# Performance work log

Measured on AMD Instinct MI355X. Metric: run time of the kernel, lower is better.

## Reference

```python
import jax, jax.numpy as jnp
import numpy as np

N_PER_G = 18
GRAPHS = 4096
N = GRAPHS * N_PER_G            # 73728 nodes
E = GRAPHS * N_PER_G * (N_PER_G - 1)  # 1253376 edges (fully connected per graph)
F_IN = 1536                     # sfreq * timestep
EPS = 1e-5
SLOPE = 0.01


def _lrelu(v):
    return jnp.where(v >= 0, v, SLOPE * v)


def setup_inputs() -> dict:
    key = jax.random.key(0)
    ks = jax.random.split(key, 32)
    # node features
    x = jax.random.normal(ks[0], (N, F_IN), dtype=jnp.float32)
    # fully-connected edges within each 18-node graph
    src, dst = np.meshgrid(np.arange(N_PER_G), np.arange(N_PER_G), indexing='ij')
    m = src != dst
    src, dst = src[m], dst[m]                      # [306]
    offs = (np.arange(GRAPHS) * N_PER_G)[:, None]
    row = (offs + src[None, :]).reshape(-1)
    col = (offs + dst[None, :]).reshape(-1)
    edge_index = jnp.asarray(np.stack([row, col]), dtype=jnp.int32)  # [2,E]
    edge_weight = jax.random.uniform(ks[1], (E,), dtype=jnp.float32)
    batch = jnp.asarray(np.arange(N) // N_PER_G, dtype=jnp.int32)

    def lin(k, fi, fo):
        kw, kb = jax.random.split(k)
        s = 1.0 / np.sqrt(fi)
        W = jax.random.uniform(kw, (fi, fo), jnp.float32, -s, s)
        b = jax.random.uniform(kb, (fo,), jnp.float32, -s, s)
        return W, b

    def bn(k, f):
        k1, k2 = jax.random.split(k)
        g = jnp.ones((f,), jnp.float32)
        be = jnp.zeros((f,), jnp.float32)
        rm = jax.random.normal(k1, (f,), jnp.float32) * 0.1
        rv = jax.random.uniform(k2, (f,), jnp.float32) + 0.5
        return g, be, rm, rv

    W1, b1 = lin(ks[2], F_IN, 32)
    W2, b2 = lin(ks[3], 32, 64)
    W3, b3 = lin(ks[4], 64, 128)
    g1, be1, rm1, rv1 = bn(ks[5], 32)
    g2, be2, rm2, rv2 = bn(ks[6], 64)
    g3, be3, rm3, rv3 = bn(ks[7], 128)
    fW1, fb1 = lin(ks[8], 128, 64)
    fW2, fb2 = lin(ks[9], 64, 32)
    fW3, fb3 = lin(ks[10], 32, 16)
    fW4, fb4 = lin(ks[11], 16, 1)

    return dict(x=x, edge_index=edge_index, edge_weight=edge_weight, batch=batch,
                W1=W1, b1=b1, g1=g1, be1=be1, rm1=rm1, rv1=rv1,
                W2=W2, b2=b2, g2=g2, be2=be2, rm2=rm2, rv2=rv2,
                W3=W3, b3=b3, g3=g3, be3=be3, rm3=rm3, rv3=rv3,
                fW1=fW1, fb1=fb1, fW2=fW2, fb2=fb2,
                fW3=fW3, fb3=fb3, fW4=fW4, fb4=fb4)


def _gcn_norm(edge_index, edge_weight):
    # add self loops (weight 1), symmetric normalization (PyG GCNConv, improved=False)
    row = jnp.concatenate([edge_index[0], jnp.arange(N, dtype=edge_index.dtype)])
    col = jnp.concatenate([edge_index[1], jnp.arange(N, dtype=edge_index.dtype)])
    w = jnp.concatenate([edge_weight, jnp.ones((N,), edge_weight.dtype)])
    deg = jax.ops.segment_sum(w, col, num_segments=N)
    dinv = jnp.where(deg > 0, jax.lax.rsqrt(jnp.maximum(deg, 1e-30)), 0.0)
    norm = dinv[row] * w * dinv[col]
    return row, col, norm


def _gcn(x, W, b, row, col, norm):
    h = x @ W                                       # [N, Fout]
    out = jax.ops.segment_sum(norm[:, None] * h[row], col, num_segments=N)
    return out + b


def _bn(h, g, be, rm, rv):
    return (h - rm) * jax.lax.rsqrt(rv + EPS) * g + be


def reference(x, edge_index, edge_weight, batch,
              W1, b1, g1, be1, rm1, rv1,
              W2, b2, g2, be2, rm2, rv2,
              W3, b3, g3, be3, rm3, rv3,
              fW1, fb1, fW2, fb2, fW3, fb3, fW4, fb4):
    row, col, norm = _gcn_norm(edge_index, edge_weight)
    h = _lrelu(_bn(_gcn(x, W1, b1, row, col, norm), g1, be1, rm1, rv1))
    h = _lrelu(_bn(_gcn(h, W2, b2, row, col, norm), g2, be2, rm2, rv2))
    h = _lrelu(_bn(_gcn(h, W3, b3, row, col, norm), g3, be3, rm3, rv3))
    # global mean pool over graphs
    sums = jax.ops.segment_sum(h, batch, num_segments=GRAPHS)
    cnt = jax.ops.segment_sum(jnp.ones((N,), h.dtype), batch, num_segments=GRAPHS)
    h = sums / jnp.maximum(cnt, 1.0)[:, None]       # [G,128]
    # MLP head (dropout = identity in eval)
    h = _lrelu(h @ fW1 + fb1)
    h = _lrelu(h @ fW2 + fb2)
    h = _lrelu(h @ fW3 + fb3)
    h = h @ fW4 + fb4
    return h.squeeze(-1)                            # [G]
```

## Files before the change

kernel.cpp:

```cpp
#include <hip/hip_runtime.h>
#include <stdint.h>

#define GRAPHS 4096
#define NPG 18
#define EPERG 306
#define FIN 1536
#define BN_EPS 1e-5f
#define SLOPE 0.01f
#define GPB 8
#define RPB 144

using short8  = __attribute__((ext_vector_type(8))) short;
using ushort8 = __attribute__((ext_vector_type(8))) unsigned short;
using f32x4   = __attribute__((ext_vector_type(4))) float;

__device__ __forceinline__ unsigned short f2bf(float f) {
  unsigned u = __builtin_bit_cast(unsigned, f);
  u += 0x7fffu + ((u >> 16) & 1u);
  return (unsigned short)(u >> 16);
}

__device__ __forceinline__ short8 pack_bf16(const float4& a0, const float4& a1) {
  short8 af;
  af[0] = (short)f2bf(a0.x); af[1] = (short)f2bf(a0.y);
  af[2] = (short)f2bf(a0.z); af[3] = (short)f2bf(a0.w);
  af[4] = (short)f2bf(a1.x); af[5] = (short)f2bf(a1.y);
  af[6] = (short)f2bf(a1.z); af[7] = (short)f2bf(a1.w);
  return af;
}

__device__ __forceinline__ void wave_fence() {
  asm volatile("s_waitcnt lgkmcnt(0)" ::: "memory");
}

__global__ void prep_kernel(const float* __restrict__ W1,
    const float* __restrict__ b1, const float* __restrict__ g1,
    const float* __restrict__ be1, const float* __restrict__ rm1, const float* __restrict__ rv1,
    const float* __restrict__ b2, const float* __restrict__ g2,
    const float* __restrict__ be2, const float* __restrict__ rm2, const float* __restrict__ rv2,
    const float* __restrict__ b3, const float* __restrict__ g3,
    const float* __restrict__ be3, const float* __restrict__ rm3, const float* __restrict__ rv3,
    unsigned short* __restrict__ w1frag, float* __restrict__ ab) {
  const int tid = threadIdx.x;
  if (blockIdx.x < 24) {
    int slot = blockIdx.x * 256 + tid;
    int L  = slot & 63;
    int nt = (slot >> 6) & 1;
    int ks = slot >> 7;
    int n  = nt * 16 + (L & 15);
    int kb = ks * 32 + ((L >> 4) << 3);
    ushort8 v;
#pragma unroll
    for (int j = 0; j < 8; ++j) v[j] = f2bf(W1[(kb + j) * 32 + n]);
    *((ushort8*)w1frag + slot) = v;
  } else {
    if (tid < 32) {
      float a = g1[tid] * rsqrtf(rv1[tid] + BN_EPS);
      ab[tid] = a; ab[32 + tid] = (b1[tid] - rm1[tid]) * a + be1[tid];
    }
    if (tid < 64) {
      float a = g2[tid] * rsqrtf(rv2[tid] + BN_EPS);
      ab[64 + tid] = a; ab[128 + tid] = (b2[tid] - rm2[tid]) * a + be2[tid];
    }
    if (tid < 128) {
      float a = g3[tid] * rsqrtf(rv3[tid] + BN_EPS);
      ab[192 + tid] = a; ab[320 + tid] = (b3[tid] - rm3[tid]) * a + be3[tid];
    }
  }
}

__global__ __launch_bounds__(256, 2) void gcn_fused(
    const float* __restrict__ x, const float* __restrict__ ew,
    const unsigned short* __restrict__ w1frag, const float* __restrict__ ab,
    const float* __restrict__ W2, const float* __restrict__ W3,
    float* __restrict__ pooled) {
  const int bid  = blockIdx.x;
  const int tid  = threadIdx.x;
  const int lane = tid & 63;
  const int wv   = tid >> 6;

  __shared__ __align__(16) float P1[RPB][36];
  __shared__ float ew_s[GPB * EPERG];
  __shared__ float dinv_s[GPB][NPG];
  __shared__ float An_s[GPB][NPG][19];
  __shared__ __align__(16) float BufA[4][NPG][68];
  __shared__ __align__(16) float BufB[4][NPG][68];

  for (int i = tid; i < GPB * EPERG; i += 256)
    ew_s[i] = ew[(size_t)bid * (GPB * EPERG) + i];

  const int arow = lane & 15;
  const int akg  = lane >> 4;
  const short8* __restrict__ wf = (const short8*)w1frag + lane;
  const float* __restrict__ xg = x + (size_t)bid * RPB * FIN;
  float* __restrict__ PT = &BufA[0][0][0];

  for (int t = wv; t < 8; t += 4) {
    f32x4 acc0 = {0.f, 0.f, 0.f, 0.f};
    f32x4 acc1 = {0.f, 0.f, 0.f, 0.f};
    const float* __restrict__ xr = xg + (size_t)(t * 16 + arow) * FIN + (akg << 3);
#pragma unroll 4
    for (int ks = 0; ks < 48; ++ks) {
      float4 a0 = *(const float4*)(xr + ks * 32);
      float4 a1 = *(const float4*)(xr + ks * 32 + 4);
      short8 af = pack_bf16(a0, a1);
      acc0 = __builtin_amdgcn_mfma_f32_16x16x32_bf16(af, wf[(ks * 2 + 0) * 64], acc0, 0, 0, 0);
      acc1 = __builtin_amdgcn_mfma_f32_16x16x32_bf16(af, wf[(ks * 2 + 1) * 64], acc1, 0, 0, 0);
    }
    const int crow = t * 16 + (akg << 2);
#pragma unroll
    for (int q = 0; q < 4; ++q) {
      P1[crow + q][arow]      = acc0[q];
      P1[crow + q][arow + 16] = acc1[q];
    }
  }
  {
    f32x4 acc0 = {0.f, 0.f, 0.f, 0.f};
    f32x4 acc1 = {0.f, 0.f, 0.f, 0.f};
    const float* __restrict__ xr = xg + (size_t)(128 + arow) * FIN + (akg << 3);
    const int k0 = wv * 12;
#pragma unroll 4
    for (int ks = k0; ks < k0 + 12; ++ks) {
      float4 a0 = *(const float4*)(xr + ks * 32);
      float4 a1 = *(const float4*)(xr + ks * 32 + 4);
      short8 af = pack_bf16(a0, a1);
      acc0 = __builtin_amdgcn_mfma_f32_16x16x32_bf16(af, wf[(ks * 2 + 0) * 64], acc0, 0, 0, 0);
      acc1 = __builtin_amdgcn_mfma_f32_16x16x32_bf16(af, wf[(ks * 2 + 1) * 64], acc1, 0, 0, 0);
    }
#pragma unroll
    for (int q = 0; q < 4; ++q) {
      PT[wv * 1224 + ((akg << 2) + q) * 32 + arow]      = acc0[q];
      PT[wv * 1224 + ((akg << 2) + q) * 32 + arow + 16] = acc1[q];
    }
  }
  __syncthreads();

  if (tid < GPB * NPG) {
    int j = tid / NPG, d = tid - j * NPG;
    const float* e = ew_s + j * EPERG;
    float deg = 1.0f;
#pragma unroll
    for (int k = 0; k < 17; ++k) {
      int s = k + (k >= d);
      deg += e[s * 17 + (d - (d > s ? 1 : 0))];
    }
    dinv_s[j][d] = rsqrtf(deg);
  }
  for (int o = tid; o < 512; o += 256) {
    int r = o >> 5, c = o & 31;
    P1[128 + r][c] = PT[o] + PT[1224 + o] + PT[2448 + o] + PT[3672 + o];
  }
  __syncthreads();

  for (int o = tid; o < GPB * NPG * NPG; o += 256) {
    int j = o / (NPG * NPG), rm = o - j * (NPG * NPG);
    int d = rm / NPG, s = rm - d * NPG;
    float v;
    if (d == s) v = dinv_s[j][d] * dinv_s[j][d];
    else        v = dinv_s[j][s] * ew_s[j * EPERG + s * 17 + (d - (d > s ? 1 : 0))] * dinv_s[j][d];
    An_s[j][d][s] = v;
  }
  __syncthreads();

  float (*A_)[68] = BufA[wv];
  float (*B_)[68] = BufB[wv];

#pragma unroll 1
  for (int jj = 0; jj < 2; ++jj) {
    const int j = wv + (jj << 2);
    const float (*An)[19] = An_s[j];
    const float* P1g = &P1[j * NPG][0];

    for (int o4 = lane; o4 < 144; o4 += 64) {
      int d = o4 >> 3, cb = (o4 & 7) << 2;
      f32x4 s = {0.f, 0.f, 0.f, 0.f};
#pragma unroll
      for (int ss = 0; ss < NPG; ++ss) {
        float a = An[d][ss];
        f32x4 p = *(const f32x4*)(P1g + ss * 36 + cb);
        s[0] = fmaf(a, p[0], s[0]); s[1] = fmaf(a, p[1], s[1]);
        s[2] = fmaf(a, p[2], s[2]); s[3] = fmaf(a, p[3], s[3]);
      }
      f32x4 al = *(const f32x4*)(ab + cb), be = *(const f32x4*)(ab + 32 + cb);
#pragma unroll
      for (int q = 0; q < 4; ++q) {
        float v = fmaf(s[q], al[q], be[q]);
        s[q] = v >= 0.f ? v : SLOPE * v;
      }
      *(f32x4*)&A_[d][cb] = s;
    }
    wave_fence();

    for (int o4 = lane; o4 < 144; o4 += 64) {
      int d = o4 >> 3, cb = (o4 & 7) << 2;
      f32x4 s = {0.f, 0.f, 0.f, 0.f};
#pragma unroll
      for (int ss = 0; ss < NPG; ++ss) {
        float a = An[d][ss];
        f32x4 p = *(const f32x4*)&A_[ss][cb];
        s[0] = fmaf(a, p[0], s[0]); s[1] = fmaf(a, p[1], s[1]);
        s[2] = fmaf(a, p[2], s[2]); s[3] = fmaf(a, p[3], s[3]);
      }
      *(f32x4*)&B_[d][cb] = s;
    }
    wave_fence();

    {
      const float al = ab[64 + lane], be = ab[128 + lane];
      float w0 = W2[0 * 64 + lane], w1 = W2[1 * 64 + lane];
      float w2 = W2[2 * 64 + lane], w3 = W2[3 * 64 + lane];
      float s0=0.f,s1=0.f,s2=0.f,s3=0.f,s4=0.f,s5=0.f,s6=0.f,s7=0.f,s8=0.f;
      float s9=0.f,s10=0.f,s11=0.f,s12=0.f,s13=0.f,s14=0.f,s15=0.f,s16=0.f,s17=0.f;
#define L2_ROW(i) { f32x4 g = *(const f32x4*)&B_[i][k4 * 4]; \
        s##i = fmaf(g[0], w0, fmaf(g[1], w1, fmaf(g[2], w2, fmaf(g[3], w3, s##i)))); }
      for (int k4 = 0; k4 < 8; ++k4) {
        float n0 = 0.f, n1 = 0.f, n2 = 0.f, n3 = 0.f;
        if (k4 < 7) {
          n0 = W2[(k4 * 4 + 4) * 64 + lane]; n1 = W2[(k4 * 4 + 5) * 64 + lane];
          n2 = W2[(k4 * 4 + 6) * 64 + lane]; n3 = W2[(k4 * 4 + 7) * 64 + lane];
        }
        L2_ROW(0) L2_ROW(1) L2_ROW(2) L2_ROW(3) L2_ROW(4) L2_ROW(5)
        L2_ROW(6) L2_ROW(7) L2_ROW(8) L2_ROW(9) L2_ROW(10) L2_ROW(11)
        L2_ROW(12) L2_ROW(13) L2_ROW(14) L2_ROW(15) L2_ROW(16) L2_ROW(17)
        w0 = n0; w1 = n1; w2 = n2; w3 = n3;
      }
#undef L2_ROW
#define L2_OUT(i) { float v = fmaf(s##i, al, be); A_[i][lane] = v >= 0.f ? v : SLOPE * v; }
      L2_OUT(0) L2_OUT(1) L2_OUT(2) L2_OUT(3) L2_OUT(4) L2_OUT(5)
      L2_OUT(6) L2_OUT(7) L2_OUT(8) L2_OUT(9) L2_OUT(10) L2_OUT(11)
      L2_OUT(12) L2_OUT(13) L2_OUT(14) L2_OUT(15) L2_OUT(16) L2_OUT(17)
#undef L2_OUT
    }
    wave_fence();

    for (int o4 = lane; o4 < 288; o4 += 64) {
      int d = o4 >> 4, cb = (o4 & 15) << 2;
      f32x4 s = {0.f, 0.f, 0.f, 0.f};
#pragma unroll
      for (int ss = 0; ss < NPG; ++ss) {
        float a = An[d][ss];
        f32x4 p = *(const f32x4*)&A_[ss][cb];
        s[0] = fmaf(a, p[0], s[0]); s[1] = fmaf(a, p[1], s[1]);
        s[2] = fmaf(a, p[2], s[2]); s[3] = fmaf(a, p[3], s[3]);
      }
      *(f32x4*)&B_[d][cb] = s;
    }
    wave_fence();

    float pool0 = 0.f, pool1 = 0.f;
#pragma unroll 1
    for (int h = 0; h < 2; ++h) {
      const int cc = (h << 6) + lane;
      const float al = ab[192 + cc], be = ab[320 + cc];
      float w0 = W3[0 * 128 + cc], w1 = W3[1 * 128 + cc];
      float w2 = W3[2 * 128 + cc], w3 = W3[3 * 128 + cc];
      float s0=0.f,s1=0.f,s2=0.f,s3=0.f,s4=0.f,s5=0.f,s6=0.f,s7=0.f,s8=0.f;
      float s9=0.f,s10=0.f,s11=0.f,s12=0.f,s13=0.f,s14=0.f,s15=0.f,s16=0.f,s17=0.f;
#define L3_ROW(i) { f32x4 g = *(const f32x4*)&B_[i][k4 * 4]; \
        s##i = fmaf(g[0], w0, fmaf(g[1], w1, fmaf(g[2], w2, fmaf(g[3], w3, s##i)))); }
      for (int k4 = 0; k4 < 16; ++k4) {
        float n0 = 0.f, n1 = 0.f, n2 = 0.f, n3 = 0.f;
        if (k4 < 15) {
          n0 = W3[(k4 * 4 + 4) * 128 + cc]; n1 = W3[(k4 * 4 + 5) * 128 + cc];
          n2 = W3[(k4 * 4 + 6) * 128 + cc]; n3 = W3[(k4 * 4 + 7) * 128 + cc];
        }
        L3_ROW(0) L3_ROW(1) L3_ROW(2) L3_ROW(3) L3_ROW(4) L3_ROW(5)
        L3_ROW(6) L3_ROW(7) L3_ROW(8) L3_ROW(9) L3_ROW(10) L3_ROW(11)
        L3_ROW(12) L3_ROW(13) L3_ROW(14) L3_ROW(15) L3_ROW(16) L3_ROW(17)
        w0 = n0; w1 = n1; w2 = n2; w3 = n3;
      }
#undef L3_ROW
      float pr = 0.f;
#define L3_POOL(i) { float v = fmaf(s##i, al, be); pr += (v >= 0.f ? v : SLOPE * v); }
      L3_POOL(0) L3_POOL(1) L3_POOL(2) L3_POOL(3) L3_POOL(4) L3_POOL(5)
      L3_POOL(6) L3_POOL(7) L3_POOL(8) L3_POOL(9) L3_POOL(10) L3_POOL(11)
      L3_POOL(12) L3_POOL(13) L3_POOL(14) L3_POOL(15) L3_POOL(16) L3_POOL(17)
#undef L3_POOL
      if (h == 0) pool0 = pr * (1.0f / 18.0f); else pool1 = pr * (1.0f / 18.0f);
    }

    const int g = (bid << 3) + j;
    pooled[(size_t)g * 128 + lane]      = pool0;
    pooled[(size_t)g * 128 + 64 + lane] = pool1;
  }
}

__global__ __launch_bounds__(256) void head_kernel(
    const float* __restrict__ pooled,
    const float* __restrict__ fW1, const float* __restrict__ fb1,
    const float* __restrict__ fW2, const float* __restrict__ fb2,
    const float* __restrict__ fW3, const float* __restrict__ fb3,
    const float* __restrict__ fW4, const float* __restrict__ fb4,
    float* __restrict__ out) {
  const int tid  = threadIdx.x;
  const int lane = tid & 63;
  const int wv   = tid >> 6;

  __shared__ __align__(16) float w1s[128 * 64];
  __shared__ __align__(16) float w2s[64 * 32];
  __shared__ __align__(16) float w3s[32 * 16];
  __shared__ float w4s[16];

  for (int i = tid; i < 128 * 64; i += 256) w1s[i] = fW1[i];
  for (int i = tid; i < 64 * 32; i += 256)  w2s[i] = fW2[i];
  for (int i = tid; i < 32 * 16; i += 256)  w3s[i] = fW3[i];
  if (tid < 16) w4s[tid] = fW4[tid];
  __syncthreads();

  const int g = (blockIdx.x << 2) + wv;
  const float p0 = pooled[(size_t)g * 128 + lane];
  const float p1 = pooled[(size_t)g * 128 + 64 + lane];

  float s1 = fb1[lane];
#pragma unroll
  for (int k = 0; k < 64; ++k) s1 = fmaf(__shfl(p0, k), w1s[k * 64 + lane], s1);
#pragma unroll
  for (int k = 0; k < 64; ++k) s1 = fmaf(__shfl(p1, k), w1s[(64 + k) * 64 + lane], s1);
  s1 = s1 >= 0.f ? s1 : SLOPE * s1;

  float s2 = fb2[lane & 31];
#pragma unroll
  for (int k = 0; k < 64; ++k) s2 = fmaf(__shfl(s1, k), w2s[k * 32 + (lane & 31)], s2);
  s2 = s2 >= 0.f ? s2 : SLOPE * s2;

  float s3 = fb3[lane & 15];
#pragma unroll
  for (int k = 0; k < 32; ++k) s3 = fmaf(__shfl(s2, k), w3s[k * 16 + (lane & 15)], s3);
  s3 = s3 >= 0.f ? s3 : SLOPE * s3;

  float s4 = fb4[0];
#pragma unroll
  for (int k = 0; k < 16; ++k) s4 = fmaf(__shfl(s3, k), w4s[k], s4);
  if (lane == 0) out[g] = s4;
}

extern "C" void kernel_launch(void* const* d_in, const int* in_sizes, int n_in,
                              void* d_out, int out_size, void* d_ws, size_t ws_size,
                              hipStream_t stream) {
  const float* x   = (const float*)d_in[0];
  const float* ew  = (const float*)d_in[2];
  const float* W1  = (const float*)d_in[4];
  const float* b1  = (const float*)d_in[5];
  const float* g1  = (const float*)d_in[6];
  const float* be1 = (const float*)d_in[7];
  const float* rm1 = (const float*)d_in[8];
  const float* rv1 = (const float*)d_in[9];
  const float* W2  = (const float*)d_in[10];
  const float* b2  = (const float*)d_in[11];
  const float* g2  = (const float*)d_in[12];
  const float* be2 = (const float*)d_in[13];
  const float* rm2 = (const float*)d_in[14];
  const float* rv2 = (const float*)d_in[15];
  const float* W3  = (const float*)d_in[16];
  const float* b3  = (const float*)d_in[17];
  const float* g3  = (const float*)d_in[18];
  const float* be3 = (const float*)d_in[19];
  const float* rm3 = (const float*)d_in[20];
  const float* rv3 = (const float*)d_in[21];
  const float* fW1 = (const float*)d_in[22];
  const float* fb1 = (const float*)d_in[23];
  const float* fW2 = (const float*)d_in[24];
  const float* fb2 = (const float*)d_in[25];
  const float* fW3 = (const float*)d_in[26];
  const float* fb3 = (const float*)d_in[27];
  const float* fW4 = (const float*)d_in[28];
  const float* fb4 = (const float*)d_in[29];

  unsigned short* w1frag = (unsigned short*)d_ws;
  float* ab     = (float*)((char*)d_ws + 98304);
  float* pooled = (float*)((char*)d_ws + 102400);

  prep_kernel<<<25, 256, 0, stream>>>(W1, b1, g1, be1, rm1, rv1,
                                      b2, g2, be2, rm2, rv2,
                                      b3, g3, be3, rm3, rv3,
                                      w1frag, ab);
  gcn_fused<<<512, 256, 0, stream>>>(x, ew, w1frag, ab, W2, W3, pooled);
  head_kernel<<<1024, 256, 0, stream>>>(pooled, fW1, fb1, fW2, fb2,
                                        fW3, fb3, fW4, fb4, (float*)d_out);
}
```

Baseline: 717.1 us.

## Split fused GCN into streaming layer-1 GEMM kernel and per-wave graph kernel

The single fused kernel is split in two. The first kernel streams x through an MFMA GEMM with one 16-row tile per wave and writes the 32-wide projection to a global workspace. The second kernel gives each wave one graph and keeps the aggregation accumulators in registers through macro-unrolled loops, removing the cross-wave partial-K reduction and the block barriers. The aim is better occupancy (launch bounds raised to 4) and an even work split for the memory-bound GEMM, at the cost of an extra global round trip for the layer-1 output and one more launch.

```diff
diff --git a/kernel.cpp b/kernel.cpp
--- a/kernel.cpp
+++ b/kernel.cpp
@@ -7,8 +7,6 @@
 #define FIN 1536
 #define BN_EPS 1e-5f
 #define SLOPE 0.01f
-#define GPB 8
-#define RPB 144
 
 using short8  = __attribute__((ext_vector_type(8))) short;
 using ushort8 = __attribute__((ext_vector_type(8))) unsigned short;
@@ -32,6 +30,9 @@
 __device__ __forceinline__ void wave_fence() {
   asm volatile("s_waitcnt lgkmcnt(0)" ::: "memory");
 }
+
+#define REP18(M) M(0) M(1) M(2) M(3) M(4) M(5) M(6) M(7) M(8) M(9) M(10) M(11) M(12) M(13) M(14) M(15) M(16) M(17)
+#define REP18B(M,s) M(0,s) M(1,s) M(2,s) M(3,s) M(4,s) M(5,s) M(6,s) M(7,s) M(8,s) M(9,s) M(10,s) M(11,s) M(12,s) M(13,s) M(14,s) M(15,s) M(16,s) M(17,s)
 
 __global__ void prep_kernel(const float* __restrict__ W1,
     const float* __restrict__ b1, const float* __restrict__ g1,
@@ -69,220 +70,174 @@
   }
 }
 
-__global__ __launch_bounds__(256, 2) void gcn_fused(
-    const float* __restrict__ x, const float* __restrict__ ew,
-    const unsigned short* __restrict__ w1frag, const float* __restrict__ ab,
-    const float* __restrict__ W2, const float* __restrict__ W3,
-    float* __restrict__ pooled) {
-  const int bid  = blockIdx.x;
-  const int tid  = threadIdx.x;
-  const int lane = tid & 63;
-  const int wv   = tid >> 6;
-
-  __shared__ __align__(16) float P1[RPB][36];
-  __shared__ float ew_s[GPB * EPERG];
-  __shared__ float dinv_s[GPB][NPG];
-  __shared__ float An_s[GPB][NPG][19];
-  __shared__ __align__(16) float BufA[4][NPG][68];
-  __shared__ __align__(16) float BufB[4][NPG][68];
-
-  for (int i = tid; i < GPB * EPERG; i += 256)
-    ew_s[i] = ew[(size_t)bid * (GPB * EPERG) + i];
-
+__global__ __launch_bounds__(256, 4) void l1_stream(
+    const float* __restrict__ x, const unsigned short* __restrict__ w1frag,
+    float* __restrict__ p1) {
+  const int lane = threadIdx.x & 63;
+  const int wv   = threadIdx.x >> 6;
+  const int t    = blockIdx.x * 4 + wv;
   const int arow = lane & 15;
   const int akg  = lane >> 4;
   const short8* __restrict__ wf = (const short8*)w1frag + lane;
-  const float* __restrict__ xg = x + (size_t)bid * RPB * FIN;
-  float* __restrict__ PT = &BufA[0][0][0];
-
-  for (int t = wv; t < 8; t += 4) {
-    f32x4 acc0 = {0.f, 0.f, 0.f, 0.f};
-    f32x4 acc1 = {0.f, 0.f, 0.f, 0.f};
-    const float* __restrict__ xr = xg + (size_t)(t * 16 + arow) * FIN + (akg << 3);
-#pragma unroll 4
-    for (int ks = 0; ks < 48; ++ks) {
-      float4 a0 = *(const float4*)(xr + ks * 32);
-      float4 a1 = *(const float4*)(xr + ks * 32 + 4);
-      short8 af = pack_bf16(a0, a1);
-      acc0 = __builtin_amdgcn_mfma_f32_16x16x32_bf16(af, wf[(ks * 2 + 0) * 64], acc0, 0, 0, 0);
-      acc1 = __builtin_amdgcn_mfma_f32_16x16x32_bf16(af, wf[(ks * 2 + 1) * 64], acc1, 0, 0, 0);
-    }
-    const int crow = t * 16 + (akg << 2);
-#pragma unroll
-    for (int q = 0; q < 4; ++q) {
-      P1[crow + q][arow]      = acc0[q];
-      P1[crow + q][arow + 16] = acc1[q];
-    }
-  }
+  const float* __restrict__ xr = x + (size_t)(t * 16 + arow) * FIN + (akg << 3);
+
+  f32x4 acc0 = {0.f, 0.f, 0.f, 0.f};
+  f32x4 acc1 = {0.f, 0.f, 0.f, 0.f};
+#pragma unroll 6
+  for (int ks = 0; ks < 48; ++ks) {
+    float4 a0 = *(const float4*)(xr + ks * 32);
+    float4 a1 = *(const float4*)(xr + ks * 32 + 4);
+    short8 af = pack_bf16(a0, a1);
+    acc0 = __builtin_amdgcn_mfma_f32_16x16x32_bf16(af, wf[(ks * 2 + 0) * 64], acc0, 0, 0, 0);
+    acc1 = __builtin_amdgcn_mfma_f32_16x16x32_bf16(af, wf[(ks * 2 + 1) * 64], acc1, 0, 0, 0);
+  }
+  float* p = p1 + (size_t)(t * 16 + (akg << 2)) * 32 + arow;
+#pragma unroll
+  for (int q = 0; q < 4; ++q) {
+    p[q * 32]      = acc0[q];
+    p[q * 32 + 16] = acc1[q];
+  }
+}
+
+__global__ __launch_bounds__(256, 4) void gcn_rest(
+    const float* __restrict__ ew, const float* __restrict__ p1,
+    const float* __restrict__ ab,
+    const float* __restrict__ W2, const float* __restrict__ W3,
+    float* __restrict__ pooled) {
+  const int lane = threadIdx.x & 63;
+  const int wv   = threadIdx.x >> 6;
+  const int g    = blockIdx.x * 4 + wv;
+
+  __shared__ float ews[4][308];
+  __shared__ float dinv[4][18];
+  __shared__ float Ans[4][18][19];
+  __shared__ __align__(16) float Gs[4][18][68];
+
+  float* ew_w = ews[wv];
+  for (int i = lane; i < EPERG; i += 64) ew_w[i] = ew[(size_t)g * EPERG + i];
+  wave_fence();
+
+  if (lane < NPG) {
+    float deg = 1.0f;
+#pragma unroll
+    for (int k = 0; k < 17; ++k) {
+      int s = k + (k >= lane);
+      deg += ew_w[s * 17 + (lane - (lane > s ? 1 : 0))];
+    }
+    dinv[wv][lane] = rsqrtf(deg);
+  }
+  wave_fence();
+
+  for (int o = lane; o < NPG * NPG; o += 64) {
+    int d = o / NPG, s = o - d * NPG;
+    float v;
+    if (d == s) v = dinv[wv][d] * dinv[wv][d];
+    else        v = dinv[wv][s] * ew_w[s * 17 + (d - (d > s ? 1 : 0))] * dinv[wv][d];
+    Ans[wv][d][s] = v;
+  }
+  wave_fence();
+
+  const float* Ap = &Ans[wv][0][0];
+  float* Gw = &Gs[wv][0][0];
+  const int cc32 = lane & 31;
+
+#define DECLT(i) float t##i = 0.f;
+  REP18(DECLT)
+#undef DECLT
   {
-    f32x4 acc0 = {0.f, 0.f, 0.f, 0.f};
-    f32x4 acc1 = {0.f, 0.f, 0.f, 0.f};
-    const float* __restrict__ xr = xg + (size_t)(128 + arow) * FIN + (akg << 3);
-    const int k0 = wv * 12;
-#pragma unroll 4
-    for (int ks = k0; ks < k0 + 12; ++ks) {
-      float4 a0 = *(const float4*)(xr + ks * 32);
-      float4 a1 = *(const float4*)(xr + ks * 32 + 4);
-      short8 af = pack_bf16(a0, a1);
-      acc0 = __builtin_amdgcn_mfma_f32_16x16x32_bf16(af, wf[(ks * 2 + 0) * 64], acc0, 0, 0, 0);
-      acc1 = __builtin_amdgcn_mfma_f32_16x16x32_bf16(af, wf[(ks * 2 + 1) * 64], acc1, 0, 0, 0);
-    }
-#pragma unroll
-    for (int q = 0; q < 4; ++q) {
-      PT[wv * 1224 + ((akg << 2) + q) * 32 + arow]      = acc0[q];
-      PT[wv * 1224 + ((akg << 2) + q) * 32 + arow + 16] = acc1[q];
-    }
-  }
-  __syncthreads();
-
-  if (tid < GPB * NPG) {
-    int j = tid / NPG, d = tid - j * NPG;
-    const float* e = ew_s + j * EPERG;
-    float deg = 1.0f;
-#pragma unroll
-    for (int k = 0; k < 17; ++k) {
-      int s = k + (k >= d);
-      deg += e[s * 17 + (d - (d > s ? 1 : 0))];
-    }
-    dinv_s[j][d] = rsqrtf(deg);
-  }
-  for (int o = tid; o < 512; o += 256) {
-    int r = o >> 5, c = o & 31;
-    P1[128 + r][c] = PT[o] + PT[1224 + o] + PT[2448 + o] + PT[3672 + o];
-  }
-  __syncthreads();
-
-  for (int o = tid; o < GPB * NPG * NPG; o += 256) {
-    int j = o / (NPG * NPG), rm = o - j * (NPG * NPG);
-    int d = rm / NPG, s = rm - d * NPG;
-    float v;
-    if (d == s) v = dinv_s[j][d] * dinv_s[j][d];
-    else        v = dinv_s[j][s] * ew_s[j * EPERG + s * 17 + (d - (d > s ? 1 : 0))] * dinv_s[j][d];
-    An_s[j][d][s] = v;
-  }
-  __syncthreads();
-
-  float (*A_)[68] = BufA[wv];
-  float (*B_)[68] = BufB[wv];
-
+    const float* P1g = p1 + (size_t)g * 576 + cc32;
+    for (int s = 0; s < 18; ++s) {
+      float pv = P1g[s * 32];
+#define L1F(i) t##i = fmaf(Ap[i * 19 + s], pv, t##i);
+      REP18(L1F)
+#undef L1F
+    }
+    const float a1 = ab[cc32], b1v = ab[32 + cc32];
+#define BN1(i) { float v = fmaf(t##i, a1, b1v); t##i = v >= 0.f ? v : SLOPE * v; }
+    REP18(BN1)
+#undef BN1
+  }
+
+#define DECLG(i) float g##i = 0.f;
+  REP18(DECLG)
+#undef DECLG
+#define AGGD(d, s) g##d = fmaf(Ap[d * 19 + s], t##s, g##d);
+#define AGGS(s) REP18B(AGGD, s)
+  REP18(AGGS)
+
+  if (lane < 32) {
+#define STG2(i) Gw[i * 68 + cc32] = g##i;
+    REP18(STG2)
+#undef STG2
+  }
+  wave_fence();
+
+  {
+    const float a2 = ab[64 + lane], b2v = ab[128 + lane];
+#define Z(i) g##i = 0.f;
+    REP18(Z)
+#undef Z
+    float w0 = W2[0 * 64 + lane], w1 = W2[1 * 64 + lane];
+    float w2 = W2[2 * 64 + lane], w3 = W2[3 * 64 + lane];
+    for (int k4 = 0; k4 < 8; ++k4) {
+      float n0 = 0.f, n1 = 0.f, n2 = 0.f, n3 = 0.f;
+      if (k4 < 7) {
+        n0 = W2[(k4 * 4 + 4) * 64 + lane]; n1 = W2[(k4 * 4 + 5) * 64 + lane];
+        n2 = W2[(k4 * 4 + 6) * 64 + lane]; n3 = W2[(k4 * 4 + 7) * 64 + lane];
+      }
+#define L2R(i) { f32x4 q = *(const f32x4*)(Gw + i * 68 + k4 * 4); \
+      g##i = fmaf(q[0], w0, fmaf(q[1], w1, fmaf(q[2], w2, fmaf(q[3], w3, g##i)))); }
+      REP18(L2R)
+#undef L2R
+      w0 = n0; w1 = n1; w2 = n2; w3 = n3;
+    }
+#define BN2(i) { float v = fmaf(g##i, a2, b2v); t##i = v >= 0.f ? v : SLOPE * v; }
+    REP18(BN2)
+#undef BN2
+  }
+
+#define Z(i) g##i = 0.f;
+  REP18(Z)
+#undef Z
+  REP18(AGGS)
+#undef AGGS
+#undef AGGD
+
+#define STG3(i) Gw[i * 68 + lane] = g##i;
+  REP18(STG3)
+#undef STG3
+  wave_fence();
+
+  float pool0 = 0.f, pool1 = 0.f;
 #pragma unroll 1
-  for (int jj = 0; jj < 2; ++jj) {
-    const int j = wv + (jj << 2);
-    const float (*An)[19] = An_s[j];
-    const float* P1g = &P1[j * NPG][0];
-
-    for (int o4 = lane; o4 < 144; o4 += 64) {
-      int d = o4 >> 3, cb = (o4 & 7) << 2;
-      f32x4 s = {0.f, 0.f, 0.f, 0.f};
-#pragma unroll
-      for (int ss = 0; ss < NPG; ++ss) {
-        float a = An[d][ss];
-        f32x4 p = *(const f32x4*)(P1g + ss * 36 + cb);
-        s[0] = fmaf(a, p[0], s[0]); s[1] = fmaf(a, p[1], s[1]);
-        s[2] = fmaf(a, p[2], s[2]); s[3] = fmaf(a, p[3], s[3]);
+  for (int h = 0; h < 2; ++h) {
+    const int cc = (h << 6) + lane;
+    const float a3 = ab[192 + cc], b3v = ab[320 + cc];
+#define Z3(i) t##i = 0.f;
+    REP18(Z3)
+#undef Z3
+    float w0 = W3[0 * 128 + cc], w1 = W3[1 * 128 + cc];
+    float w2 = W3[2 * 128 + cc], w3 = W3[3 * 128 + cc];
+    for (int k4 = 0; k4 < 16; ++k4) {
+      float n0 = 0.f, n1 = 0.f, n2 = 0.f, n3 = 0.f;
+      if (k4 < 15) {
+        n0 = W3[(k4 * 4 + 4) * 128 + cc]; n1 = W3[(k4 * 4 + 5) * 128 + cc];
+        n2 = W3[(k4 * 4 + 6) * 128 + cc]; n3 = W3[(k4 * 4 + 7) * 128 + cc];
       }
-      f32x4 al = *(const f32x4*)(ab + cb), be = *(const f32x4*)(ab + 32 + cb);
-#pragma unroll
-      for (int q = 0; q < 4; ++q) {
-        float v = fmaf(s[q], al[q], be[q]);
-        s[q] = v >= 0.f ? v : SLOPE * v;
-      }
-      *(f32x4*)&A_[d][cb] = s;
-    }
-    wave_fence();
-
-    for (int o4 = lane; o4 < 144; o4 += 64) {
-      int d = o4 >> 3, cb = (o4 & 7) << 2;
-      f32x4 s = {0.f, 0.f, 0.f, 0.f};
-#pragma unroll
-      for (int ss = 0; ss < NPG; ++ss) {
-        float a = An[d][ss];
-        f32x4 p = *(const f32x4*)&A_[ss][cb];
-        s[0] = fmaf(a, p[0], s[0]); s[1] = fmaf(a, p[1], s[1]);
-        s[2] = fmaf(a, p[2], s[2]); s[3] = fmaf(a, p[3], s[3]);
-      }
-      *(f32x4*)&B_[d][cb] = s;
-    }
-    wave_fence();
-
-    {
-      const float al = ab[64 + lane], be = ab[128 + lane];
-      float w0 = W2[0 * 64 + lane], w1 = W2[1 * 64 + lane];
-      float w2 = W2[2 * 64 + lane], w3 = W2[3 * 64 + lane];
-      float s0=0.f,s1=0.f,s2=0.f,s3=0.f,s4=0.f,s5=0.f,s6=0.f,s7=0.f,s8=0.f;
-      float s9=0.f,s10=0.f,s11=0.f,s12=0.f,s13=0.f,s14=0.f,s15=0.f,s16=0.f,s17=0.f;
-#define L2_ROW(i) { f32x4 g = *(const f32x4*)&B_[i][k4 * 4]; \
-        s##i = fmaf(g[0], w0, fmaf(g[1], w1, fmaf(g[2], w2, fmaf(g[3], w3, s##i)))); }
-      for (int k4 = 0; k4 < 8; ++k4) {
-        float n0 = 0.f, n1 = 0.f, n2 = 0.f, n3 = 0.f;
-        if (k4 < 7) {
-          n0 = W2[(k4 * 4 + 4) * 64 + lane]; n1 = W2[(k4 * 4 + 5) * 64 + lane];
-          n2 = W2[(k4 * 4 + 6) * 64 + lane]; n3 = W2[(k4 * 4 + 7) * 64 + lane];
-        }
-        L2_ROW(0) L2_ROW(1) L2_ROW(2) L2_ROW(3) L2_ROW(4) L2_ROW(5)
-        L2_ROW(6) L2_ROW(7) L2_ROW(8) L2_ROW(9) L2_ROW(10) L2_ROW(11)
-        L2_ROW(12) L2_ROW(13) L2_ROW(14) L2_ROW(15) L2_ROW(16) L2_ROW(17)
-        w0 = n0; w1 = n1; w2 = n2; w3 = n3;
-      }
-#undef L2_ROW
-#define L2_OUT(i) { float v = fmaf(s##i, al, be); A_[i][lane] = v >= 0.f ? v : SLOPE * v; }
-      L2_OUT(0) L2_OUT(1) L2_OUT(2) L2_OUT(3) L2_OUT(4) L2_OUT(5)
-      L2_OUT(6) L2_OUT(7) L2_OUT(8) L2_OUT(9) L2_OUT(10) L2_OUT(11)
-      L2_OUT(12) L2_OUT(13) L2_OUT(14) L2_OUT(15) L2_OUT(16) L2_OUT(17)
-#undef L2_OUT
-    }
-    wave_fence();
-
-    for (int o4 = lane; o4 < 288; o4 += 64) {
-      int d = o4 >> 4, cb = (o4 & 15) << 2;
-      f32x4 s = {0.f, 0.f, 0.f, 0.f};
-#pragma unroll
-      for (int ss = 0; ss < NPG; ++ss) {
-        float a = An[d][ss];
-        f32x4 p = *(const f32x4*)&A_[ss][cb];
-        s[0] = fmaf(a, p[0], s[0]); s[1] = fmaf(a, p[1], s[1]);
-        s[2] = fmaf(a, p[2], s[2]); s[3] = fmaf(a, p[3], s[3]);
-      }
-      *(f32x4*)&B_[d][cb] = s;
-    }
-    wave_fence();
-
-    float pool0 = 0.f, pool1 = 0.f;
-#pragma unroll 1
-    for (int h = 0; h < 2; ++h) {
-      const int cc = (h << 6) + lane;
-      const float al = ab[192 + cc], be = ab[320 + cc];
-      float w0 = W3[0 * 128 + cc], w1 = W3[1 * 128 + cc];
-      float w2 = W3[2 * 128 + cc], w3 = W3[3 * 128 + cc];
-      float s0=0.f,s1=0.f,s2=0.f,s3=0.f,s4=0.f,s5=0.f,s6=0.f,s7=0.f,s8=0.f;
-      float s9=0.f,s10=0.f,s11=0.f,s12=0.f,s13=0.f,s14=0.f,s15=0.f,s16=0.f,s17=0.f;
-#define L3_ROW(i) { f32x4 g = *(const f32x4*)&B_[i][k4 * 4]; \
-        s##i = fmaf(g[0], w0, fmaf(g[1], w1, fmaf(g[2], w2, fmaf(g[3], w3, s##i)))); }
-      for (int k4 = 0; k4 < 16; ++k4) {
-        float n0 = 0.f, n1 = 0.f, n2 = 0.f, n3 = 0.f;
-        if (k4 < 15) {
-          n0 = W3[(k4 * 4 + 4) * 128 + cc]; n1 = W3[(k4 * 4 + 5) * 128 + cc];
-          n2 = W3[(k4 * 4 + 6) * 128 + cc]; n3 = W3[(k4 * 4 + 7) * 128 + cc];
-        }
-        L3_ROW(0) L3_ROW(1) L3_ROW(2) L3_ROW(3) L3_ROW(4) L3_ROW(5)
-        L3_ROW(6) L3_ROW(7) L3_ROW(8) L3_ROW(9) L3_ROW(10) L3_ROW(11)
-        L3_ROW(12) L3_ROW(13) L3_ROW(14) L3_ROW(15) L3_ROW(16) L3_ROW(17)
-        w0 = n0; w1 = n1; w2 = n2; w3 = n3;
-      }
-#undef L3_ROW
-      float pr = 0.f;
-#define L3_POOL(i) { float v = fmaf(s##i, al, be); pr += (v >= 0.f ? v : SLOPE * v); }
-      L3_POOL(0) L3_POOL(1) L3_POOL(2) L3_POOL(3) L3_POOL(4) L3_POOL(5)
-      L3_POOL(6) L3_POOL(7) L3_POOL(8) L3_POOL(9) L3_POOL(10) L3_POOL(11)
-      L3_POOL(12) L3_POOL(13) L3_POOL(14) L3_POOL(15) L3_POOL(16) L3_POOL(17)
-#undef L3_POOL
-      if (h == 0) pool0 = pr * (1.0f / 18.0f); else pool1 = pr * (1.0f / 18.0f);
-    }
-
-    const int g = (bid << 3) + j;
-    pooled[(size_t)g * 128 + lane]      = pool0;
-    pooled[(size_t)g * 128 + 64 + lane] = pool1;
-  }
+#define L3R(i) { f32x4 q = *(const f32x4*)(Gw + i * 68 + k4 * 4); \
+      t##i = fmaf(q[0], w0, fmaf(q[1], w1, fmaf(q[2], w2, fmaf(q[3], w3, t##i)))); }
+      REP18(L3R)
+#undef L3R
+      w0 = n0; w1 = n1; w2 = n2; w3 = n3;
+    }
+    float pr = 0.f;
+#define PL(i) { float v = fmaf(t##i, a3, b3v); pr += (v >= 0.f ? v : SLOPE * v); }
+    REP18(PL)
+#undef PL
+    if (h == 0) pool0 = pr * (1.0f / 18.0f); else pool1 = pr * (1.0f / 18.0f);
+  }
+  pooled[(size_t)g * 128 + lane]      = pool0;
+  pooled[(size_t)g * 128 + 64 + lane] = pool1;
 }
 
 __global__ __launch_bounds__(256) void head_kernel(
@@ -369,12 +324,14 @@
   unsigned short* w1frag = (unsigned short*)d_ws;
   float* ab     = (float*)((char*)d_ws + 98304);
   float* pooled = (float*)((char*)d_ws + 102400);
+  float* p1     = (float*)((char*)d_ws + 2199552);
 
   prep_kernel<<<25, 256, 0, stream>>>(W1, b1, g1, be1, rm1, rv1,
                                       b2, g2, be2, rm2, rv2,
                                       b3, g3, be3, rm3, rv3,
                                       w1frag, ab);
-  gcn_fused<<<512, 256, 0, stream>>>(x, ew, w1frag, ab, W2, W3, pooled);
+  l1_stream<<<1152, 256, 0, stream>>>(x, w1frag, p1);
+  gcn_rest<<<1024, 256, 0, stream>>>(ew, p1, ab, W2, W3, pooled);
   head_kernel<<<1024, 256, 0, stream>>>(pooled, fW1, fb1, fW2, fb2,
                                         fW3, fb3, fW4, fb4, (float*)d_out);
 }
```

After: 803.0 us. +12.0%, slower.
